# Kernel optimization log

Measured on AMD Instinct MI355X. Metric: run time of the kernel, lower is better.

Reference implementation:

```python
import jax, jax.numpy as jnp
import numpy as np

B, N, C = 256, 256, 128   # batch (=N_res rows), seq len, pair channels
H, D = 4, 128             # heads, per-head dim (== output_dim per module code)
O = 128                   # output_dim


def _glorot(key, shape, fan_in, fan_out):
    limit = np.sqrt(6.0 / (fan_in + fan_out))
    return jax.random.uniform(key, shape, jnp.float32, -limit, limit)


def setup_inputs() -> dict:
    key = jax.random.key(0)
    ks = jax.random.split(key, 9)
    q_data = jax.random.normal(ks[0], (B, N, C), jnp.float32)
    m_data = jax.random.normal(ks[1], (B, N, C), jnp.float32)
    bias = jax.random.normal(ks[2], (B, 1, N, N), jnp.float32)
    nonbatched_bias = jax.random.normal(ks[3], (H, N, N), jnp.float32)
    query_w = _glorot(ks[4], (C, H, D), C, H * D)
    key_w = _glorot(ks[5], (C, H, D), C, H * D)
    value_w = _glorot(ks[6], (C, H, D), C, H * D)
    gating_w = jnp.zeros((C, H, D), jnp.float32)
    gating_b = jnp.ones((H, D), jnp.float32)
    output_w = _glorot(ks[7], (H, D, O), H * D, O)
    output_b = jnp.zeros((O,), jnp.float32)
    return {
        'q_data': q_data, 'm_data': m_data, 'bias': bias,
        'nonbatched_bias': nonbatched_bias,
        'query_w': query_w, 'key_w': key_w, 'value_w': value_w,
        'gating_w': gating_w, 'gating_b': gating_b,
        'output_w': output_w, 'output_b': output_b,
    }


def reference(q_data, m_data, bias, nonbatched_bias,
              query_w, key_w, value_w, gating_w, gating_b,
              output_w, output_b):
    key_dim = query_w.shape[-1]  # per-head dim (tied to output_dim in module)
    q = jnp.einsum('bqa,ahc->bqhc', q_data, query_w) * key_dim ** (-0.5)
    k = jnp.einsum('bka,ahc->bkhc', m_data, key_w)
    v = jnp.einsum('bka,ahc->bkhc', m_data, value_w)
    logits = jnp.einsum('bqhc,bkhc->bhqk', q, k) + bias
    logits = logits + nonbatched_bias[None]  # broadcast shared bias over batch
    weights = jax.nn.softmax(logits, axis=-1)
    weighted_avg = jnp.einsum('bhqk,bkhc->bqhc', weights, v)
    gate = jax.nn.sigmoid(jnp.einsum('bqc,chv->bqhv', q_data, gating_w) + gating_b)
    weighted_avg = weighted_avg * gate
    return jnp.einsum('bqhc,hco->bqo', weighted_avg, output_w) + output_b
```

## Files before the change

### kernel.cpp

```cpp
#include <hip/hip_runtime.h>
#include <stdint.h>


typedef unsigned short u16;
typedef u16 u16x8 __attribute__((ext_vector_type(8)));
typedef u16 u16x4 __attribute__((ext_vector_type(4)));
typedef __bf16 bf16x8 __attribute__((ext_vector_type(8)));
typedef float floatx4 __attribute__((ext_vector_type(4)));

union B8 { u16x8 u; bf16x8 b; };

__device__ __forceinline__ float bf2f(u16 u) {
  union { uint32_t i; float f; } v; v.i = ((uint32_t)u) << 16; return v.f;
}
__device__ __forceinline__ u16 f2bf(float f) {
  union { float f; uint32_t i; } v; v.f = f;
  return (u16)((v.i + 0x7fffu + ((v.i >> 16) & 1u)) >> 16);
}
__device__ __forceinline__ bf16x8 ld8(const u16* p) { return *(const bf16x8*)p; }
__device__ __forceinline__ floatx4 mfma16(bf16x8 a, bf16x8 b, floatx4 c) {
  return __builtin_amdgcn_mfma_f32_16x16x32_bf16(a, b, c, 0, 0, 0);
}
__device__ __forceinline__ void cfence() { asm volatile("" ::: "memory"); }

template<bool BF>
__device__ __forceinline__ bf16x8 ldin8(const void* p, long long idx) {
  if constexpr (BF) {
    return *(const bf16x8*)((const u16*)p + idx);
  } else {
    const float* f = (const float*)p + idx;
    floatx4 a = *(const floatx4*)f;
    floatx4 b = *(const floatx4*)(f + 4);
    B8 r;
    #pragma unroll
    for (int i = 0; i < 4; ++i) { r.u[i] = f2bf(a[i]); r.u[i + 4] = f2bf(b[i]); }
    return r.b;
  }
}
template<bool BF>
__device__ __forceinline__ float ldin1(const void* p, long long idx) {
  if constexpr (BF) return bf2f(((const u16*)p)[idx]);
  else              return ((const float*)p)[idx];
}

template<bool BF>
__device__ __forceinline__ void pre_body(
    const void* nbias,
    const void* qw, const void* kw, const void* vw, const void* gw,
    const void* ow, u16* wt, u16* nb16)
{
  const int blk = blockIdx.x, tid = threadIdx.x;
  if (blk < 64) {
    long long base = (long long)blk * 4096;
    #pragma unroll
    for (int it = 0; it < 4; ++it) {
      long long idx = base + it * 1024 + tid * 4;
      if constexpr (BF) {
        *(u16x4*)(nb16 + idx) = *(const u16x4*)((const u16*)nbias + idx);
      } else {
        floatx4 v = *(const floatx4*)((const float*)nbias + idx);
        u16x4 o;
        #pragma unroll
        for (int i = 0; i < 4; ++i) o[i] = f2bf(v[i]);
        *(u16x4*)(nb16 + idx) = o;
      }
    }
  } else if (blk < 80) {
    const int mh = blk - 64, mat = mh >> 2, h = mh & 3;
    const void* W = (mat == 0) ? qw : (mat == 1) ? kw : (mat == 2) ? vw : gw;
    u16* dst = wt + mh * 16384;
    for (int idx = tid; idx < 16384; idx += 256) {
      int c = idx >> 7, d = idx & 127;
      dst[d * 128 + c] = f2bf(ldin1<BF>(W, (long long)c * 512 + h * 128 + d));
    }
  } else {
    const int part = blk - 80;
    u16* dst = wt + 16 * 16384;
    for (int idx = tid; idx < 16384; idx += 256) {
      int k = idx >> 7, o = idx & 127;
      int kg = part * 128 + k;
      dst[o * 512 + kg] = f2bf(ldin1<BF>(ow, (long long)kg * 128 + o));
    }
  }
}

__global__ __launch_bounds__(256) void k_pre(
    const void* nbias,
    const void* qw, const void* kw, const void* vw, const void* gw,
    const void* ow, const void* gating_b, u16* wt, u16* nb16)
{
  const bool bf = (*(const uint32_t*)gating_b) == 0x3F803F80u;
  if (bf) pre_body<true >(nbias, qw, kw, vw, gw, ow, wt, nb16);
  else    pre_body<false>(nbias, qw, kw, vw, gw, ow, wt, nb16);
}

template<bool BF>
__device__ __forceinline__ void proj_body(
    const void* q_data, const void* m_data,
    const u16* wt, u16* reg, int b0, int Bc)
{
  const int tid  = threadIdx.x;
  const int lane = tid & 63, w = tid >> 6;
  const int quad = lane >> 4, l15 = lane & 15;
  const int mat  = blockIdx.y >> 2, h = blockIdx.y & 3;
  const int r0l  = blockIdx.x * 128;
  const int bl   = r0l >> 8, n0 = r0l & 255;
  const int bg   = b0 + bl;
  const long long regElems = (long long)Bc * 131072;

  const void* src = (mat == 0) ? q_data : m_data;
  const u16*  Wt  = wt + (mat * 4 + h) * 16384;

  const int wm = w >> 1, wn = w & 1;
  floatx4 acc[4][4];
  #pragma unroll
  for (int mi = 0; mi < 4; ++mi)
    #pragma unroll
    for (int ni = 0; ni < 4; ++ni)
      acc[mi][ni] = (floatx4){0.f, 0.f, 0.f, 0.f};

  #pragma unroll
  for (int ks = 0; ks < 4; ++ks) {
    bf16x8 af[4], bw[4];
    #pragma unroll
    for (int mi = 0; mi < 4; ++mi) {
      long long row = (long long)bg * 256 + n0 + wm * 64 + mi * 16 + l15;
      af[mi] = ldin8<BF>(src, row * 128 + ks * 32 + quad * 8);
    }
    #pragma unroll
    for (int ni = 0; ni < 4; ++ni) {
      int col = wn * 64 + ni * 16 + l15;
      bw[ni] = ld8(Wt + col * 128 + ks * 32 + quad * 8);
    }
    #pragma unroll
    for (int mi = 0; mi < 4; ++mi)
      #pragma unroll
      for (int ni = 0; ni < 4; ++ni)
        acc[mi][ni] = mfma16(af[mi], bw[ni], acc[mi][ni]);
  }

  const float scale = 0.088388347648318447f;
  const long long bh = (long long)(bl * 4 + h);
  #pragma unroll
  for (int mi = 0; mi < 4; ++mi) {
    #pragma unroll
    for (int ni = 0; ni < 4; ++ni) {
      if (mat == 2) {
        int j = wn * 64 + ni * 16 + l15;
        int i0 = wm * 64 + mi * 16 + quad * 4;
        u16x4 v4;
        #pragma unroll
        for (int r = 0; r < 4; ++r) v4[r] = f2bf(acc[mi][ni][r]);
        *(u16x4*)(reg + 2 * regElems + (bh * 128 + j) * 256 + (n0 + i0)) = v4;
      } else {
        #pragma unroll
        for (int r = 0; r < 4; ++r) {
          int i = wm * 64 + mi * 16 + quad * 4 + r;
          int j = wn * 64 + ni * 16 + l15;
          float v = acc[mi][ni][r];
          if (mat == 0) v *= scale;
          reg[(long long)mat * regElems + (bh * 256 + (n0 + i)) * 128 + j] = f2bf(v);
        }
      }
    }
  }
}

__global__ __launch_bounds__(256) void k_proj(
    const void* q_data, const void* m_data, const void* gating_b,
    const u16* wt, u16* reg, int b0, int Bc)
{
  const bool bf = (*(const uint32_t*)gating_b) == 0x3F803F80u;
  if (bf) proj_body<true >(q_data, m_data, wt, reg, b0, Bc);
  else    proj_body<false>(q_data, m_data, wt, reg, b0, Bc);
}

template<bool BF>
__device__ __forceinline__ void attn_body(
    const void* q_data, const void* __restrict__ bias,
    const u16* __restrict__ nb16, const void* gating_b,
    const u16* __restrict__ wt, u16* reg, int b0, int Bc, char* smem)
{
  const int tid  = threadIdx.x;
  const int lane = tid & 63, w = tid >> 6;
  const int quad = lane >> 4, l15 = lane & 15;

  const int nwg = Bc * 16;
  const int id  = blockIdx.x;
  const int per = nwg >> 3;
  const int swz = (id & 7) * per + (id >> 3);
  const int bl = swz >> 4, h = (swz >> 2) & 3, qt = swz & 3;

  const int bg = b0 + bl;
  const int m0 = qt * 64 + w * 16;
  const long long regElems = (long long)Bc * 131072;
  const long long bh = (long long)(bl * 4 + h);

  const u16* Qb = reg;
  const u16* Kb = reg + regElems     + bh * 32768;
  const u16* Vt = reg + 2 * regElems + bh * 32768;
  u16*       Ob = reg + 3 * regElems;
  const u16* wtG = wt + (3 * 4 + h) * 16384;

  char* scr = smem + w * 4352;

  bf16x8 aq[4];
  #pragma unroll
  for (int ks = 0; ks < 4; ++ks)
    aq[ks] = ld8(Qb + (bh * 256 + m0 + l15) * 128 + ks * 32 + quad * 8);

  floatx4 s[16];
  #pragma unroll
  for (int nt = 0; nt < 16; ++nt) s[nt] = (floatx4){0.f, 0.f, 0.f, 0.f};

  #pragma unroll
  for (int kc = 0; kc < 4; ++kc) {
    float* sBf = (float*)scr;
    #pragma unroll
    for (int it = 0; it < 4; ++it) {
      int slot = it * 64 + lane;
      int row = slot >> 4, c4 = (slot & 15) << 2;
      long long gi = ((long long)bg * 256 + m0 + row) * 256 + kc * 64 + c4;
      long long ni = ((long long)h  * 256 + m0 + row) * 256 + kc * 64 + c4;
      u16x4 nu = *(const u16x4*)(nb16 + ni);
      floatx4 v;
      if constexpr (BF) {
        u16x4 bu = *(const u16x4*)((const u16*)bias + gi);
        #pragma unroll
        for (int i = 0; i < 4; ++i) v[i] = bf2f(bu[i]) + bf2f(nu[i]);
      } else {
        floatx4 bv = *(const floatx4*)((const float*)bias + gi);
        #pragma unroll
        for (int i = 0; i < 4; ++i) v[i] = bv[i] + bf2f(nu[i]);
      }
      *(floatx4*)(sBf + row * 68 + c4) = v;
    }
    #pragma unroll
    for (int ntl = 0; ntl < 4; ++ntl) {
      const int nt = kc * 4 + ntl;
      #pragma unroll
      for (int ks = 0; ks < 4; ++ks) {
        bf16x8 bk = ld8(Kb + (kc * 64 + ntl * 16 + l15) * 128 + ks * 32 + quad * 8);
        s[nt] = mfma16(aq[ks], bk, s[nt]);
      }
      #pragma unroll
      for (int r = 0; r < 4; ++r)
        s[nt][r] += sBf[(quad * 4 + r) * 68 + ntl * 16 + l15];
    }
    cfence();
  }

  float mx[4] = {-1e30f, -1e30f, -1e30f, -1e30f};
  #pragma unroll
  for (int nt = 0; nt < 16; ++nt)
    #pragma unroll
    for (int r = 0; r < 4; ++r) mx[r] = fmaxf(mx[r], s[nt][r]);
  #pragma unroll
  for (int r = 0; r < 4; ++r)
    #pragma unroll
    for (int off = 1; off < 16; off <<= 1)
      mx[r] = fmaxf(mx[r], __shfl_xor(mx[r], off));
  float sm[4] = {0.f, 0.f, 0.f, 0.f};
  #pragma unroll
  for (int nt = 0; nt < 16; ++nt)
    #pragma unroll
    for (int r = 0; r < 4; ++r) {
      float e = __expf(s[nt][r] - mx[r]);
      s[nt][r] = e; sm[r] += e;
    }
  #pragma unroll
  for (int r = 0; r < 4; ++r)
    #pragma unroll
    for (int off = 1; off < 16; off <<= 1)
      sm[r] += __shfl_xor(sm[r], off);
  float inv[4];
  #pragma unroll
  for (int r = 0; r < 4; ++r) inv[r] = 1.f / sm[r];

  u16* sPw = (u16*)scr;
  floatx4 o[8];
  #pragma unroll
  for (int dt = 0; dt < 8; ++dt) o[dt] = (floatx4){0.f, 0.f, 0.f, 0.f};
  #pragma unroll
  for (int half = 0; half < 2; ++half) {
    #pragma unroll
    for (int ntl = 0; ntl < 8; ++ntl)
      #pragma unroll
      for (int r = 0; r < 4; ++r)
        sPw[(quad * 4 + r) * 136 + ntl * 16 + l15] =
            f2bf(s[half * 8 + ntl][r] * inv[r]);
    bf16x8 ap[4];
    #pragma unroll
    for (int ks = 0; ks < 4; ++ks)
      ap[ks] = ld8(sPw + l15 * 136 + ks * 32 + quad * 8);
    #pragma unroll
    for (int dt = 0; dt < 8; ++dt)
      #pragma unroll
      for (int ks = 0; ks < 4; ++ks) {
        bf16x8 bv = ld8(Vt + (dt * 16 + l15) * 256 + half * 128 + ks * 32 + quad * 8);
        o[dt] = mfma16(ap[ks], bv, o[dt]);
      }
    cfence();
  }

  bf16x8 aqd[4];
  #pragma unroll
  for (int ks = 0; ks < 4; ++ks)
    aqd[ks] = ldin8<BF>(q_data, ((long long)bg * 256 + m0 + l15) * 128 + ks * 32 + quad * 8);
  #pragma unroll
  for (int nt = 0; nt < 8; ++nt) {
    floatx4 g = (floatx4){0.f, 0.f, 0.f, 0.f};
    #pragma unroll
    for (int ks = 0; ks < 4; ++ks) {
      bf16x8 bw = ld8(wtG + (nt * 16 + l15) * 128 + ks * 32 + quad * 8);
      g = mfma16(aqd[ks], bw, g);
    }
    #pragma unroll
    for (int r = 0; r < 4; ++r) {
      int row = m0 + quad * 4 + r, d = nt * 16 + l15;
      float gate = 1.f / (1.f + __expf(-(g[r] + ldin1<BF>(gating_b, h * 128 + d))));
      Ob[(bh * 256 + row) * 128 + d] = f2bf(o[nt][r] * gate);
    }
  }
}

__global__ __launch_bounds__(256, 4) void k_attn(
    const void* q_data, const void* bias, const u16* nb16,
    const void* gating_b, const u16* wt, u16* reg, int b0, int Bc)
{
  __shared__ __align__(16) char smem[17408];
  const bool bf = (*(const uint32_t*)gating_b) == 0x3F803F80u;
  if (bf) attn_body<true >(q_data, bias, nb16, gating_b, wt, reg, b0, Bc, smem);
  else    attn_body<false>(q_data, bias, nb16, gating_b, wt, reg, b0, Bc, smem);
}

template<bool BF>
__device__ __forceinline__ void out_body(
    const u16* wsr, const u16* wtO, const void* output_b,
    void* out, int b0)
{
  const int tid  = threadIdx.x;
  const int lane = tid & 63, w = tid >> 6;
  const int quad = lane >> 4, l15 = lane & 15;
  const int wm = w >> 1, wn = w & 1;
  const int r0l = blockIdx.x * 32;
  const int bl  = r0l >> 8, n0 = r0l & 255;

  floatx4 acc[4];
  #pragma unroll
  for (int ni = 0; ni < 4; ++ni) acc[ni] = (floatx4){0.f, 0.f, 0.f, 0.f};

  #pragma unroll
  for (int kt = 0; kt < 4; ++kt) {
    #pragma unroll
    for (int ks = 0; ks < 4; ++ks) {
      bf16x8 af = ld8(wsr + ((long long)(bl * 4 + kt) * 256 + n0 + wm * 16 + l15) * 128
                          + ks * 32 + quad * 8);
      #pragma unroll
      for (int ni = 0; ni < 4; ++ni) {
        int col = wn * 64 + ni * 16 + l15;
        bf16x8 bw = ld8(wtO + (long long)col * 512 + kt * 128 + ks * 32 + quad * 8);
        acc[ni] = mfma16(af, bw, acc[ni]);
      }
    }
  }

  #pragma unroll
  for (int ni = 0; ni < 4; ++ni) {
    #pragma unroll
    for (int r = 0; r < 4; ++r) {
      int i = wm * 16 + quad * 4 + r;
      int j = wn * 64 + ni * 16 + l15;
      long long orow = (long long)b0 * 256 + r0l + i;
      float v = acc[ni][r] + ldin1<BF>(output_b, j);
      if constexpr (BF) ((u16*)out)[orow * 128 + j] = f2bf(v);
      else              ((float*)out)[orow * 128 + j] = v;
    }
  }
}

__global__ __launch_bounds__(256) void k_out(
    const u16* wsr, const u16* wtO, const void* output_b,
    const void* gating_b, void* out, int b0)
{
  const bool bf = (*(const uint32_t*)gating_b) == 0x3F803F80u;
  if (bf) out_body<true >(wsr, wtO, output_b, out, b0);
  else    out_body<false>(wsr, wtO, output_b, out, b0);
}

extern "C" void kernel_launch(void* const* d_in, const int* in_sizes, int n_in,
                              void* d_out, int out_size, void* d_ws, size_t ws_size,
                              hipStream_t stream)
{
  (void)in_sizes; (void)n_in; (void)out_size;
  const void* q_data   = d_in[0];
  const void* m_data   = d_in[1];
  const void* bias     = d_in[2];
  const void* nbias    = d_in[3];
  const void* query_w  = d_in[4];
  const void* key_w    = d_in[5];
  const void* value_w  = d_in[6];
  const void* gating_w = d_in[7];
  const void* gating_b = d_in[8];
  const void* output_w = d_in[9];
  const void* output_b = d_in[10];
  u16* ws = (u16*)d_ws;

  const long long wtElems  = 16 * 16384 + 128 * 512;
  const long long nbElems  = 4LL * 256 * 256;
  const long long fixedElems = wtElems + nbElems;
  u16* wt   = ws;
  u16* wtO  = wt + 16 * 16384;
  u16* nb16 = ws + wtElems;
  u16* reg  = ws + fixedElems;

  const size_t per_batch_bytes = 4ull * 131072 * 2;
  const size_t fixed_bytes = (size_t)fixedElems * 2;
  int Bc = 1;
  while (Bc * 2 <= 256 &&
         fixed_bytes + (size_t)(Bc * 2) * per_batch_bytes <= ws_size) Bc *= 2;

  k_pre<<<84, 256, 0, stream>>>(nbias, query_w, key_w, value_w,
                                gating_w, output_w, gating_b, wt, nb16);

  const long long regElems = (long long)Bc * 131072;
  for (int b0 = 0; b0 < 256; b0 += Bc) {
    dim3 g1(2 * Bc, 12);
    k_proj<<<g1, 256, 0, stream>>>(q_data, m_data, gating_b, wt, reg, b0, Bc);
    k_attn<<<Bc * 16, 256, 0, stream>>>(q_data, bias, nb16, gating_b, wt,
                                        reg, b0, Bc);
    dim3 g3(8 * Bc);
    k_out<<<g3, 256, 0, stream>>>(reg + 3 * regElems, wtO, output_b,
                                  gating_b, d_out, b0);
  }
}
```

Measured before the change: 769.3 us.

## Stage K/V tiles into LDS with double-buffered async global_load_lds

The attention kernel now copies K and V chunks into two swizzled LDS buffers with global_load_lds, prefetching the next chunk while MFMAs consume the current one. It also hoists the bias loads ahead of the QK MFMAs. Previously each wave read K and V directly from global memory, and all four waves of a block re-read the same tiles. In exchange, LDS grows to about 49KB, launch bounds drop to 3 blocks per CU, and a block-wide barrier is added per chunk.

```diff
diff --git a/kernel.cpp b/kernel.cpp
--- a/kernel.cpp
+++ b/kernel.cpp
@@ -22,6 +22,12 @@
   return __builtin_amdgcn_mfma_f32_16x16x32_bf16(a, b, c, 0, 0, 0);
 }
 __device__ __forceinline__ void cfence() { asm volatile("" ::: "memory"); }
+
+__device__ __forceinline__ void gload16(const u16* g, u16* l) {
+  __builtin_amdgcn_global_load_lds(
+      (const __attribute__((address_space(1))) void*)g,
+      (__attribute__((address_space(3))) void*)l, 16, 0, 0);
+}
 
 template<bool BF>
 __device__ __forceinline__ bf16x8 ldin8(const void* p, long long idx) {
@@ -184,6 +190,7 @@
   const int tid  = threadIdx.x;
   const int lane = tid & 63, w = tid >> 6;
   const int quad = lane >> 4, l15 = lane & 15;
+  const int l7   = l15 & 7;
 
   const int nwg = Bc * 16;
   const int id  = blockIdx.x;
@@ -202,7 +209,29 @@
   u16*       Ob = reg + 3 * regElems;
   const u16* wtG = wt + (3 * 4 + h) * 16384;
 
-  char* scr = smem + w * 4352;
+  u16* kv0 = (u16*)smem;
+  u16* kv1 = kv0 + 8192;
+  char* scr = smem + 32768 + w * 4352;
+
+  auto stageK = [&](u16* dst, int kc) {
+    const u16* g = Kb + kc * 8192;
+    #pragma unroll
+    for (int it = 0; it < 4; ++it) {
+      const int rl = w * 16 + it * 4 + quad;
+      const int so = (l15 * 8) ^ ((((it * 4 + quad) & 7)) << 3);
+      gload16(g + rl * 128 + so, dst + w * 2048 + it * 512);
+    }
+  };
+  auto stageV = [&](u16* dst, int vc) {
+    const int half = vc >> 1, dc = vc & 1;
+    const u16* g = Vt + dc * 64 * 256 + half * 128;
+    #pragma unroll
+    for (int it = 0; it < 4; ++it) {
+      const int rl = w * 16 + it * 4 + quad;
+      const int so = (l15 * 8) ^ ((((it * 4 + quad) & 7)) << 3);
+      gload16(g + rl * 256 + so, dst + w * 2048 + it * 512);
+    }
+  };
 
   bf16x8 aq[4];
   #pragma unroll
@@ -213,41 +242,62 @@
   #pragma unroll
   for (int nt = 0; nt < 16; ++nt) s[nt] = (floatx4){0.f, 0.f, 0.f, 0.f};
 
+  stageK(kv0, 0);
+  __syncthreads();
+
   #pragma unroll
   for (int kc = 0; kc < 4; ++kc) {
-    float* sBf = (float*)scr;
+    u16* cur = (kc & 1) ? kv1 : kv0;
+    u16* nxt = (kc & 1) ? kv0 : kv1;
+    if (kc < 3) stageK(nxt, kc + 1);
+    else        stageV(nxt, 0);
+
+    u16x4 bb[4]; floatx4 fb[4]; u16x4 nn[4];
     #pragma unroll
     for (int it = 0; it < 4; ++it) {
-      int slot = it * 64 + lane;
-      int row = slot >> 4, c4 = (slot & 15) << 2;
+      int row = it * 4 + quad, c4 = l15 << 2;
       long long gi = ((long long)bg * 256 + m0 + row) * 256 + kc * 64 + c4;
       long long ni = ((long long)h  * 256 + m0 + row) * 256 + kc * 64 + c4;
-      u16x4 nu = *(const u16x4*)(nb16 + ni);
+      nn[it] = *(const u16x4*)(nb16 + ni);
+      if constexpr (BF) bb[it] = *(const u16x4*)((const u16*)bias + gi);
+      else              fb[it] = *(const floatx4*)((const float*)bias + gi);
+    }
+
+    #pragma unroll
+    for (int ntl = 0; ntl < 4; ++ntl) {
+      const int nt = kc * 4 + ntl;
+      #pragma unroll
+      for (int ks = 0; ks < 4; ++ks) {
+        bf16x8 bk = ld8(cur + (ntl * 16 + l15) * 128 +
+                        ((ks * 32 + quad * 8) ^ (l7 << 3)));
+        s[nt] = mfma16(aq[ks], bk, s[nt]);
+      }
+    }
+
+    float* sBf = (float*)scr;
+    #pragma unroll
+    for (int it = 0; it < 4; ++it) {
+      int row = it * 4 + quad, c4 = l15 << 2;
       floatx4 v;
       if constexpr (BF) {
-        u16x4 bu = *(const u16x4*)((const u16*)bias + gi);
-        #pragma unroll
-        for (int i = 0; i < 4; ++i) v[i] = bf2f(bu[i]) + bf2f(nu[i]);
+        #pragma unroll
+        for (int i = 0; i < 4; ++i) v[i] = bf2f(bb[it][i]) + bf2f(nn[it][i]);
       } else {
-        floatx4 bv = *(const floatx4*)((const float*)bias + gi);
-        #pragma unroll
-        for (int i = 0; i < 4; ++i) v[i] = bv[i] + bf2f(nu[i]);
+        #pragma unroll
+        for (int i = 0; i < 4; ++i) v[i] = fb[it][i] + bf2f(nn[it][i]);
       }
       *(floatx4*)(sBf + row * 68 + c4) = v;
     }
+    cfence();
     #pragma unroll
     for (int ntl = 0; ntl < 4; ++ntl) {
       const int nt = kc * 4 + ntl;
       #pragma unroll
-      for (int ks = 0; ks < 4; ++ks) {
-        bf16x8 bk = ld8(Kb + (kc * 64 + ntl * 16 + l15) * 128 + ks * 32 + quad * 8);
-        s[nt] = mfma16(aq[ks], bk, s[nt]);
-      }
-      #pragma unroll
       for (int r = 0; r < 4; ++r)
         s[nt][r] += sBf[(quad * 4 + r) * 68 + ntl * 16 + l15];
     }
     cfence();
+    __syncthreads();
   }
 
   float mx[4] = {-1e30f, -1e30f, -1e30f, -1e30f};
@@ -281,26 +331,37 @@
   floatx4 o[8];
   #pragma unroll
   for (int dt = 0; dt < 8; ++dt) o[dt] = (floatx4){0.f, 0.f, 0.f, 0.f};
-  #pragma unroll
-  for (int half = 0; half < 2; ++half) {
-    #pragma unroll
-    for (int ntl = 0; ntl < 8; ++ntl)
-      #pragma unroll
-      for (int r = 0; r < 4; ++r)
-        sPw[(quad * 4 + r) * 136 + ntl * 16 + l15] =
-            f2bf(s[half * 8 + ntl][r] * inv[r]);
-    bf16x8 ap[4];
-    #pragma unroll
-    for (int ks = 0; ks < 4; ++ks)
-      ap[ks] = ld8(sPw + l15 * 136 + ks * 32 + quad * 8);
-    #pragma unroll
-    for (int dt = 0; dt < 8; ++dt)
+  bf16x8 ap[4];
+  #pragma unroll
+  for (int vc = 0; vc < 4; ++vc) {
+    u16* cur = (vc & 1) ? kv1 : kv0;
+    u16* nxt = (vc & 1) ? kv0 : kv1;
+    if (vc < 3) stageV(nxt, vc + 1);
+    if ((vc & 1) == 0) {
+      const int half = vc >> 1;
+      #pragma unroll
+      for (int ntl = 0; ntl < 8; ++ntl)
+        #pragma unroll
+        for (int r = 0; r < 4; ++r)
+          sPw[(quad * 4 + r) * 136 + ntl * 16 + l15] =
+              f2bf(s[half * 8 + ntl][r] * inv[r]);
+      cfence();
+      #pragma unroll
+      for (int ks = 0; ks < 4; ++ks)
+        ap[ks] = ld8(sPw + l15 * 136 + ks * 32 + quad * 8);
+      cfence();
+    }
+    const int ob = (vc & 1) * 4;
+    #pragma unroll
+    for (int dtl = 0; dtl < 4; ++dtl) {
       #pragma unroll
       for (int ks = 0; ks < 4; ++ks) {
-        bf16x8 bv = ld8(Vt + (dt * 16 + l15) * 256 + half * 128 + ks * 32 + quad * 8);
-        o[dt] = mfma16(ap[ks], bv, o[dt]);
-      }
-    cfence();
+        bf16x8 bv = ld8(cur + (dtl * 16 + l15) * 128 +
+                        ((ks * 32 + quad * 8) ^ (l7 << 3)));
+        o[ob + dtl] = mfma16(ap[ks], bv, o[ob + dtl]);
+      }
+    }
+    __syncthreads();
   }
 
   bf16x8 aqd[4];
@@ -324,11 +385,11 @@
   }
 }
 
-__global__ __launch_bounds__(256, 4) void k_attn(
+__global__ __launch_bounds__(256, 3) void k_attn(
     const void* q_data, const void* bias, const u16* nb16,
     const void* gating_b, const u16* wt, u16* reg, int b0, int Bc)
 {
-  __shared__ __align__(16) char smem[17408];
+  __shared__ __align__(16) char smem[50176];
   const bool bf = (*(const uint32_t*)gating_b) == 0x3F803F80u;
   if (bf) attn_body<true >(q_data, bias, nb16, gating_b, wt, reg, b0, Bc, smem);
   else    attn_body<false>(q_data, bias, nb16, gating_b, wt, reg, b0, Bc, smem);
```

After: 684.7 us. 1.12x faster.
